# Optimization experiments

Hardware: AMD Instinct MI355X
Metric: run time of the kernel (lower is better)

Reference implementation:

```python
import jax, jax.numpy as jnp
import numpy as np


def setup_inputs() -> dict:
    key = jax.random.key(0)
    ks = jax.random.split(key, 7)
    B, C, H, W = 4, 64, 64, 64
    d = C // 8
    s = C ** -0.5  # 1x1-conv fan-in init scale
    x = jax.random.normal(ks[0], (B, C, H, W), jnp.float32)
    Wq = jax.random.normal(ks[1], (d, C), jnp.float32) * s
    bq = jnp.zeros((d,), jnp.float32)
    Wk = jax.random.normal(ks[2], (d, C), jnp.float32) * s
    bk = jnp.zeros((d,), jnp.float32)
    Wv = jax.random.normal(ks[3], (C, C), jnp.float32) * s
    bv = jnp.zeros((C,), jnp.float32)
    return {"x": x, "Wq": Wq, "bq": bq, "Wk": Wk, "bk": bk, "Wv": Wv, "bv": bv}


def reference(x, Wq, bq, Wk, bk, Wv, bv):
    B, C, H, W = x.shape
    N = H * W
    xf = x.reshape(B, C, N)                               # [B,C,N]
    # 1x1 convs == per-pixel channel matmuls
    q = jnp.einsum('dc,bcn->bnd', Wq, xf) + bq            # [B,N,d]
    k = jnp.einsum('dc,bcn->bnd', Wk, xf) + bk            # [B,N,d]
    v = jnp.einsum('ec,bcn->ben', Wv, xf) + bv[:, None]   # [B,C,N]
    # pairwise relative position offsets over flattened spatial grid
    idx = jnp.arange(N)
    col = (idx % W).astype(x.dtype)
    row = (idx // W).astype(x.dtype)
    col_diff = col[None, :] - col[:, None]                # [N,N], col_j - col_i
    row_diff = row[None, :] - row[:, None]                # [N,N]
    # scores = Q . (K + rel_pos folded into first two key channels)
    scores = jnp.einsum('bnd,bmd->bnm', q, k)             # [B,N,N]
    scores = scores + q[:, :, 0, None] * col_diff[None] + q[:, :, 1, None] * row_diff[None]
    attn = jax.nn.softmax(scores, axis=-1)                # softmax over keys
    out = jnp.einsum('bcm,bnm->bcn', v, attn)             # [B,C,N]
    return out.reshape(B, C, H, W)
```

## Files before the change

### kernel.cpp

```cpp
#include <hip/hip_runtime.h>

#define BB 4
#define CC 64
#define NN 4096

typedef __attribute__((ext_vector_type(8))) short short8;
typedef __attribute__((ext_vector_type(4))) float f32x4;
typedef __attribute__((ext_vector_type(4))) unsigned uint4v;

__device__ inline ushort f2bf(float x) {
    unsigned u = __float_as_uint(x);
    return (ushort)((u + 0x7fff + ((u >> 16) & 1)) >> 16);
}
__device__ inline float bf2f(ushort h) { return __uint_as_float(((unsigned)h) << 16); }

__device__ inline unsigned cvt_pk_bf16(float a, float b) {
    unsigned r;
    asm("v_cvt_pk_bf16_f32 %0, %1, %2" : "=v"(r) : "v"(a), "v"(b));
    return r;
}


__global__ __launch_bounds__(512) void qkv_kernel(
    const float* __restrict__ x,
    const float* __restrict__ Wq, const float* __restrict__ bq,
    const float* __restrict__ Wk, const float* __restrict__ bk,
    const float* __restrict__ Wv, const float* __restrict__ bv,
    ushort* __restrict__ qTp, ushort* __restrict__ kTp, ushort* __restrict__ vsw)
{
    __shared__ ushort vlds[32 * 68];
    const int blk = blockIdx.x;
    const int tid = threadIdx.x;

    if (blk < 32) {
        const int idx = blk * 512 + tid;
        const int b = idx >> 12, n = idx & (NN - 1);
        const float* xb = x + (size_t)b * CC * NN + n;
        float sq[8], sk[8];
#pragma unroll
        for (int d = 0; d < 8; ++d) { sq[d] = bq[d]; sk[d] = bk[d]; }
#pragma unroll 8
        for (int c = 0; c < CC; ++c) {
            const float xc = xb[c * NN];
#pragma unroll
            for (int d = 0; d < 8; ++d) {
                sq[d] += Wq[d * CC + c] * xc;
                sk[d] += Wk[d * CC + c] * xc;
            }
        }
        ushort hq[32], hk[32];
#pragma unroll
        for (int i = 0; i < 32; ++i) { hq[i] = 0; hk[i] = 0; }
#pragma unroll
        for (int d = 0; d < 8; ++d) { hq[d] = f2bf(sq[d]); hk[d] = f2bf(sk[d]); }
        hq[8]  = hq[0];
        hq[9]  = hq[1];
        hq[10] = f2bf(sq[0] - bf2f(hq[0]));
        hq[11] = f2bf(sq[1] - bf2f(hq[1]));
        const float col = (float)(n & 63), row = (float)(n >> 6);
        hk[8] = f2bf(col); hk[9] = f2bf(row); hk[10] = hk[8]; hk[11] = hk[9];

        uint4* dq = (uint4*)(qTp + (size_t)(b * NN + n) * 32);
        uint4* dk = (uint4*)(kTp + (size_t)(b * NN + n) * 32);
        const uint4* s4q = (const uint4*)hq;
        const uint4* s4k = (const uint4*)hk;
#pragma unroll
        for (int i = 0; i < 4; ++i) { dq[i] = s4q[i]; dk[i] = s4k[i]; }
        return;
    }

    const int w2 = blk - 32;
    const int bt = w2 >> 1, h = w2 & 1;
    const int b = bt >> 6, t = bt & 63;
    const int w = tid >> 6, j = tid & 63;
    const int n = t * 64 + j;
    const int e0 = __builtin_amdgcn_readfirstlane(h * 32 + w * 4);

    const float* xb = x + (size_t)b * CC * NN + n;
    float a0 = bv[e0], a1 = bv[e0 + 1], a2 = bv[e0 + 2], a3 = bv[e0 + 3];
#pragma unroll 8
    for (int c = 0; c < CC; ++c) {
        const float xc = xb[c * NN];
        a0 += Wv[(e0 + 0) * CC + c] * xc;
        a1 += Wv[(e0 + 1) * CC + c] * xc;
        a2 += Wv[(e0 + 2) * CC + c] * xc;
        a3 += Wv[(e0 + 3) * CC + c] * xc;
    }
    const int el0 = w * 4;
    vlds[(el0 + 0) * 68 + j] = f2bf(a0);
    vlds[(el0 + 1) * 68 + j] = f2bf(a1);
    vlds[(el0 + 2) * 68 + j] = f2bf(a2);
    vlds[(el0 + 3) * 68 + j] = f2bf(a3);
    __syncthreads();

    const int el = tid & 31;
    const int qd = (tid >> 5) & 3;
    const int sbh = tid >> 7;
    const int sb = sbh >> 1, hi = sbh & 1;
    const int j0 = sb * 32 + hi * 16 + qd * 4;
    const int eg = h * 32 + el;
    const uint2 val = *(const uint2*)(vlds + el * 68 + j0);
    const size_t tb = (size_t)(b * 64 + t) * 4096;
    *(uint2*)(vsw + tb + (size_t)(((sb * 4 + (eg >> 4)) * 64 + qd * 16 + (eg & 15)) * 8 + hi * 4)) = val;
}

__global__ __launch_bounds__(512) void attn_kernel(
    const ushort* __restrict__ qTp, const ushort* __restrict__ kTp,
    const ushort* __restrict__ vsw, float* __restrict__ out)
{
    const int blk = blockIdx.x;
    const int xcd = blk & 7, i8 = blk >> 3;
    const int b  = xcd >> 1;
    const int nq = (((xcd & 1) << 6) | i8) << 5;
    const int tid = threadIdx.x;
    const int wv = tid >> 6, lane = tid & 63;
    const int nn = lane & 15, quad = lane >> 4;

    __shared__ float Cb[8][1024];
    __shared__ float Mx[8][32];
    __shared__ float Db[8][32];
    __shared__ float dn[32];

    const short8 qf0 = *(const short8*)(qTp + ((size_t)(b * NN + nq + nn) * 32 + quad * 8));
    const short8 qf1 = *(const short8*)(qTp + ((size_t)(b * NN + nq + 16 + nn) * 32 + quad * 8));
    const ushort* kb = kTp + (size_t)b * NN * 32;

    float m0 = -1e30f, m1 = -1e30f;
    {
        const int t = wv * 8;
#pragma unroll
        for (int kg = 0; kg < 4; ++kg) {
            const short8 kf = *(const short8*)(kb + ((size_t)(t * 64 + kg * 16 + nn) * 32 + quad * 8));
            const f32x4 S0 = __builtin_amdgcn_mfma_f32_16x16x32_bf16(kf, qf0, (f32x4){0.f,0.f,0.f,0.f}, 0, 0, 0);
            const f32x4 S1 = __builtin_amdgcn_mfma_f32_16x16x32_bf16(kf, qf1, (f32x4){0.f,0.f,0.f,0.f}, 0, 0, 0);
            m0 = fmaxf(m0, fmaxf(fmaxf(S0[0], S0[1]), fmaxf(S0[2], S0[3])));
            m1 = fmaxf(m1, fmaxf(fmaxf(S1[0], S1[1]), fmaxf(S1[2], S1[3])));
        }
        m0 = fmaxf(m0, __shfl_xor(m0, 16, 64));
        m0 = fmaxf(m0, __shfl_xor(m0, 32, 64));
        m1 = fmaxf(m1, __shfl_xor(m1, 16, 64));
        m1 = fmaxf(m1, __shfl_xor(m1, 32, 64));
    }
    f32x4 nM0 = {-m0, -m0, -m0, -m0};
    f32x4 nM1 = {-m1, -m1, -m1, -m1};

    f32x4 acc0[4], acc1[4];
#pragma unroll
    for (int g = 0; g < 4; ++g) {
        acc0[g] = (f32x4){0.f,0.f,0.f,0.f};
        acc1[g] = (f32x4){0.f,0.f,0.f,0.f};
    }
    float dl0 = 0.f, dl1 = 0.f;

    for (int t8 = 0; t8 < 8; ++t8) {
        const int t = wv * 8 + t8;
        f32x4 s0[4], s1[4];
#pragma unroll
        for (int kg = 0; kg < 4; ++kg) {
            const short8 kf = *(const short8*)(kb + ((size_t)(t * 64 + kg * 16 + nn) * 32 + quad * 8));
            s0[kg] = __builtin_amdgcn_mfma_f32_16x16x32_bf16(kf, qf0, nM0, 0, 0, 0);
            s1[kg] = __builtin_amdgcn_mfma_f32_16x16x32_bf16(kf, qf1, nM1, 0, 0, 0);
        }
        float r0 = fmaxf(fmaxf(s0[0][0], s0[0][1]), fmaxf(s0[0][2], s0[0][3]));
        float r1 = fmaxf(fmaxf(s1[0][0], s1[0][1]), fmaxf(s1[0][2], s1[0][3]));
#pragma unroll
        for (int kg = 1; kg < 4; ++kg) {
            r0 = fmaxf(r0, fmaxf(fmaxf(s0[kg][0], s0[kg][1]), fmaxf(s0[kg][2], s0[kg][3])));
            r1 = fmaxf(r1, fmaxf(fmaxf(s1[kg][0], s1[kg][1]), fmaxf(s1[kg][2], s1[kg][3])));
        }
        r0 = fmaxf(r0, __shfl_xor(r0, 16, 64));
        r0 = fmaxf(r0, __shfl_xor(r0, 32, 64));
        r1 = fmaxf(r1, __shfl_xor(r1, 16, 64));
        r1 = fmaxf(r1, __shfl_xor(r1, 32, 64));

        if (__any((r0 > 25.f) || (r1 > 25.f))) {
            const float d0 = fmaxf(r0, 0.f), d1 = fmaxf(r1, 0.f);
            const float e0 = __expf(-d0), e1 = __expf(-d1);
            m0 += d0; m1 += d1;
            nM0 = (f32x4){-m0, -m0, -m0, -m0};
            nM1 = (f32x4){-m1, -m1, -m1, -m1};
            dl0 *= e0; dl1 *= e1;
            f32x4 e0v, e1v;
#pragma unroll
            for (int rr = 0; rr < 4; ++rr) {
                e0v[rr] = __shfl(e0, quad * 4 + rr, 64);
                e1v[rr] = __shfl(e1, quad * 4 + rr, 64);
            }
#pragma unroll
            for (int g = 0; g < 4; ++g) { acc0[g] *= e0v; acc1[g] *= e1v; }
            const f32x4 dv0 = {d0, d0, d0, d0}, dv1 = {d1, d1, d1, d1};
#pragma unroll
            for (int kg = 0; kg < 4; ++kg) { s0[kg] -= dv0; s1[kg] -= dv1; }
        }

        unsigned pw0[8], pw1[8];
#pragma unroll
        for (int kg = 0; kg < 4; ++kg) {
            const float w00 = __expf(s0[kg][0]), w01 = __expf(s0[kg][1]);
            const float w02 = __expf(s0[kg][2]), w03 = __expf(s0[kg][3]);
            const float w10 = __expf(s1[kg][0]), w11 = __expf(s1[kg][1]);
            const float w12 = __expf(s1[kg][2]), w13 = __expf(s1[kg][3]);
            dl0 += (w00 + w01) + (w02 + w03);
            dl1 += (w10 + w11) + (w12 + w13);
            pw0[2 * kg]     = cvt_pk_bf16(w00, w01);
            pw0[2 * kg + 1] = cvt_pk_bf16(w02, w03);
            pw1[2 * kg]     = cvt_pk_bf16(w10, w11);
            pw1[2 * kg + 1] = cvt_pk_bf16(w12, w13);
        }
        const uint4v u00 = {pw0[0], pw0[1], pw0[2], pw0[3]};
        const uint4v u01 = {pw0[4], pw0[5], pw0[6], pw0[7]};
        const uint4v u10 = {pw1[0], pw1[1], pw1[2], pw1[3]};
        const uint4v u11 = {pw1[4], pw1[5], pw1[6], pw1[7]};
        const short8 a00 = __builtin_bit_cast(short8, u00);
        const short8 a01 = __builtin_bit_cast(short8, u01);
        const short8 a10 = __builtin_bit_cast(short8, u10);
        const short8 a11 = __builtin_bit_cast(short8, u11);

        const ushort* vb = vsw + (size_t)(b * 64 + t) * 4096;
#pragma unroll
        for (int g = 0; g < 4; ++g) {
            const short8 vf = *(const short8*)(vb + g * 512 + lane * 8);
            acc0[g] = __builtin_amdgcn_mfma_f32_16x16x32_bf16(a00, vf, acc0[g], 0, 0, 0);
            acc1[g] = __builtin_amdgcn_mfma_f32_16x16x32_bf16(a10, vf, acc1[g], 0, 0, 0);
        }
#pragma unroll
        for (int g = 0; g < 4; ++g) {
            const short8 vf = *(const short8*)(vb + 2048 + g * 512 + lane * 8);
            acc0[g] = __builtin_amdgcn_mfma_f32_16x16x32_bf16(a01, vf, acc0[g], 0, 0, 0);
            acc1[g] = __builtin_amdgcn_mfma_f32_16x16x32_bf16(a11, vf, acc1[g], 0, 0, 0);
        }
    }

    if (quad == 0) { Mx[wv][nn] = m0; Mx[wv][16 + nn] = m1; }
    __syncthreads();
    float M0 = Mx[0][nn], M1 = Mx[0][16 + nn];
#pragma unroll
    for (int w = 1; w < 8; ++w) { M0 = fmaxf(M0, Mx[w][nn]); M1 = fmaxf(M1, Mx[w][16 + nn]); }
    const float g0 = __expf(m0 - M0), g1 = __expf(m1 - M1);
    dl0 *= g0; dl1 *= g1;
    f32x4 g0v, g1v;
#pragma unroll
    for (int rr = 0; rr < 4; ++rr) {
        g0v[rr] = __shfl(g0, quad * 4 + rr, 64);
        g1v[rr] = __shfl(g1, quad * 4 + rr, 64);
    }
#pragma unroll
    for (int g = 0; g < 4; ++g) { acc0[g] *= g0v; acc1[g] *= g1v; }

    dl0 += __shfl_xor(dl0, 16, 64); dl0 += __shfl_xor(dl0, 32, 64);
    dl1 += __shfl_xor(dl1, 16, 64); dl1 += __shfl_xor(dl1, 32, 64);
    if (quad == 0) { Db[wv][nn] = dl0; Db[wv][16 + nn] = dl1; }

#pragma unroll
    for (int g = 0; g < 4; ++g)
#pragma unroll
        for (int r = 0; r < 4; ++r)
            Cb[wv][(g * 4 + r) * 64 + lane] = acc0[g][r];
    __syncthreads();

    if (tid < 32) {
        float s = Db[0][tid];
#pragma unroll
        for (int w = 1; w < 8; ++w) s += Db[w][tid];
        dn[tid] = s;
    }
    __syncthreads();

#pragma unroll
    for (int it = 0; it < 2; ++it) {
        const int e = tid + it * 512;
        const int q = e & 15, c = e >> 4;
        const int src = ((c >> 4) * 4 + (q & 3)) * 64 + (q >> 2) * 16 + (c & 15);
        float v = Cb[0][src];
#pragma unroll
        for (int w = 1; w < 8; ++w) v += Cb[w][src];
        out[(size_t)(b * CC + c) * NN + nq + q] = v / dn[q];
    }
    __syncthreads();

#pragma unroll
    for (int g = 0; g < 4; ++g)
#pragma unroll
        for (int r = 0; r < 4; ++r)
            Cb[wv][(g * 4 + r) * 64 + lane] = acc1[g][r];
    __syncthreads();

#pragma unroll
    for (int it = 0; it < 2; ++it) {
        const int e = tid + it * 512;
        const int q = e & 15, c = e >> 4;
        const int src = ((c >> 4) * 4 + (q & 3)) * 64 + (q >> 2) * 16 + (c & 15);
        float v = Cb[0][src];
#pragma unroll
        for (int w = 1; w < 8; ++w) v += Cb[w][src];
        out[(size_t)(b * CC + c) * NN + nq + 16 + q] = v / dn[16 + q];
    }
}

extern "C" void kernel_launch(void* const* d_in, const int* in_sizes, int n_in,
                              void* d_out, int out_size, void* d_ws, size_t ws_size,
                              hipStream_t stream) {
    const float* x  = (const float*)d_in[0];
    const float* Wq = (const float*)d_in[1];
    const float* bq = (const float*)d_in[2];
    const float* Wk = (const float*)d_in[3];
    const float* bk = (const float*)d_in[4];
    const float* Wv = (const float*)d_in[5];
    const float* bv = (const float*)d_in[6];
    float* out = (float*)d_out;

    ushort* ws  = (ushort*)d_ws;
    ushort* qTp = ws;
    ushort* kTp = ws + (size_t)BB * NN * 32;
    ushort* vsw = ws + (size_t)2 * BB * NN * 32;

    qkv_kernel<<<544, 512, 0, stream>>>(x, Wq, bq, Wk, bk, Wv, bv, qTp, kTp, vsw);
    attn_kernel<<<512, 512, 0, stream>>>(qTp, kTp, vsw, out);
}
```

Baseline: 113.9 us.

## Process 64 queries per attention block to reuse K and V loads

Each attention block now handles 64 query rows (four 16-row tiles) instead of 32, and the grid is halved from 512 to 256 blocks. K and V fragments loaded per key tile are reused across twice as many query tiles, which halves global K/V traffic per query. The cost is double the accumulator registers per thread, and 256 blocks may underfill a GPU with 256 CUs running one 512-thread block each. The epilogue reductions also now run sequentially over four tiles, adding barriers.

New measurement: 111.3 us. 2.3% less time.

```diff
diff --git a/kernel.cpp b/kernel.cpp
--- a/kernel.cpp
+++ b/kernel.cpp
@@ -111,189 +111,191 @@
     const int blk = blockIdx.x;
     const int xcd = blk & 7, i8 = blk >> 3;
     const int b  = xcd >> 1;
-    const int nq = (((xcd & 1) << 6) | i8) << 5;
+    const int nq = (((xcd & 1) << 5) | i8) << 6;
     const int tid = threadIdx.x;
     const int wv = tid >> 6, lane = tid & 63;
     const int nn = lane & 15, quad = lane >> 4;
 
     __shared__ float Cb[8][1024];
-    __shared__ float Mx[8][32];
-    __shared__ float Db[8][32];
-    __shared__ float dn[32];
-
-    const short8 qf0 = *(const short8*)(qTp + ((size_t)(b * NN + nq + nn) * 32 + quad * 8));
-    const short8 qf1 = *(const short8*)(qTp + ((size_t)(b * NN + nq + 16 + nn) * 32 + quad * 8));
+    __shared__ float Mx[8][64];
+    __shared__ float Db[8][64];
+    __shared__ float dn[64];
+
+    short8 qf[4];
+#pragma unroll
+    for (int qt = 0; qt < 4; ++qt)
+        qf[qt] = *(const short8*)(qTp + ((size_t)(b * NN + nq + qt * 16 + nn) * 32 + quad * 8));
     const ushort* kb = kTp + (size_t)b * NN * 32;
 
-    float m0 = -1e30f, m1 = -1e30f;
+    float m[4] = {-1e30f, -1e30f, -1e30f, -1e30f};
     {
         const int t = wv * 8;
 #pragma unroll
-        for (int kg = 0; kg < 4; ++kg) {
-            const short8 kf = *(const short8*)(kb + ((size_t)(t * 64 + kg * 16 + nn) * 32 + quad * 8));
-            const f32x4 S0 = __builtin_amdgcn_mfma_f32_16x16x32_bf16(kf, qf0, (f32x4){0.f,0.f,0.f,0.f}, 0, 0, 0);
-            const f32x4 S1 = __builtin_amdgcn_mfma_f32_16x16x32_bf16(kf, qf1, (f32x4){0.f,0.f,0.f,0.f}, 0, 0, 0);
-            m0 = fmaxf(m0, fmaxf(fmaxf(S0[0], S0[1]), fmaxf(S0[2], S0[3])));
-            m1 = fmaxf(m1, fmaxf(fmaxf(S1[0], S1[1]), fmaxf(S1[2], S1[3])));
-        }
-        m0 = fmaxf(m0, __shfl_xor(m0, 16, 64));
-        m0 = fmaxf(m0, __shfl_xor(m0, 32, 64));
-        m1 = fmaxf(m1, __shfl_xor(m1, 16, 64));
-        m1 = fmaxf(m1, __shfl_xor(m1, 32, 64));
-    }
-    f32x4 nM0 = {-m0, -m0, -m0, -m0};
-    f32x4 nM1 = {-m1, -m1, -m1, -m1};
-
-    f32x4 acc0[4], acc1[4];
-#pragma unroll
-    for (int g = 0; g < 4; ++g) {
-        acc0[g] = (f32x4){0.f,0.f,0.f,0.f};
-        acc1[g] = (f32x4){0.f,0.f,0.f,0.f};
-    }
-    float dl0 = 0.f, dl1 = 0.f;
+        for (int p = 0; p < 2; ++p) {
+            const int q0 = 2 * p, q1 = 2 * p + 1;
+#pragma unroll
+            for (int kg = 0; kg < 4; ++kg) {
+                const short8 kf = *(const short8*)(kb + ((size_t)(t * 64 + kg * 16 + nn) * 32 + quad * 8));
+                const f32x4 S0 = __builtin_amdgcn_mfma_f32_16x16x32_bf16(kf, qf[q0], (f32x4){0.f,0.f,0.f,0.f}, 0, 0, 0);
+                const f32x4 S1 = __builtin_amdgcn_mfma_f32_16x16x32_bf16(kf, qf[q1], (f32x4){0.f,0.f,0.f,0.f}, 0, 0, 0);
+                m[q0] = fmaxf(m[q0], fmaxf(fmaxf(S0[0], S0[1]), fmaxf(S0[2], S0[3])));
+                m[q1] = fmaxf(m[q1], fmaxf(fmaxf(S1[0], S1[1]), fmaxf(S1[2], S1[3])));
+            }
+        }
+#pragma unroll
+        for (int qt = 0; qt < 4; ++qt) {
+            m[qt] = fmaxf(m[qt], __shfl_xor(m[qt], 16, 64));
+            m[qt] = fmaxf(m[qt], __shfl_xor(m[qt], 32, 64));
+        }
+    }
+    f32x4 nM[4];
+#pragma unroll
+    for (int qt = 0; qt < 4; ++qt) nM[qt] = (f32x4){-m[qt], -m[qt], -m[qt], -m[qt]};
+
+    f32x4 acc[4][4];
+#pragma unroll
+    for (int qt = 0; qt < 4; ++qt)
+#pragma unroll
+        for (int g = 0; g < 4; ++g) acc[qt][g] = (f32x4){0.f,0.f,0.f,0.f};
+    float dl[4] = {0.f, 0.f, 0.f, 0.f};
 
     for (int t8 = 0; t8 < 8; ++t8) {
         const int t = wv * 8 + t8;
-        f32x4 s0[4], s1[4];
-#pragma unroll
-        for (int kg = 0; kg < 4; ++kg) {
-            const short8 kf = *(const short8*)(kb + ((size_t)(t * 64 + kg * 16 + nn) * 32 + quad * 8));
-            s0[kg] = __builtin_amdgcn_mfma_f32_16x16x32_bf16(kf, qf0, nM0, 0, 0, 0);
-            s1[kg] = __builtin_amdgcn_mfma_f32_16x16x32_bf16(kf, qf1, nM1, 0, 0, 0);
-        }
-        float r0 = fmaxf(fmaxf(s0[0][0], s0[0][1]), fmaxf(s0[0][2], s0[0][3]));
-        float r1 = fmaxf(fmaxf(s1[0][0], s1[0][1]), fmaxf(s1[0][2], s1[0][3]));
-#pragma unroll
-        for (int kg = 1; kg < 4; ++kg) {
-            r0 = fmaxf(r0, fmaxf(fmaxf(s0[kg][0], s0[kg][1]), fmaxf(s0[kg][2], s0[kg][3])));
-            r1 = fmaxf(r1, fmaxf(fmaxf(s1[kg][0], s1[kg][1]), fmaxf(s1[kg][2], s1[kg][3])));
-        }
-        r0 = fmaxf(r0, __shfl_xor(r0, 16, 64));
-        r0 = fmaxf(r0, __shfl_xor(r0, 32, 64));
-        r1 = fmaxf(r1, __shfl_xor(r1, 16, 64));
-        r1 = fmaxf(r1, __shfl_xor(r1, 32, 64));
-
-        if (__any((r0 > 25.f) || (r1 > 25.f))) {
-            const float d0 = fmaxf(r0, 0.f), d1 = fmaxf(r1, 0.f);
-            const float e0 = __expf(-d0), e1 = __expf(-d1);
-            m0 += d0; m1 += d1;
-            nM0 = (f32x4){-m0, -m0, -m0, -m0};
-            nM1 = (f32x4){-m1, -m1, -m1, -m1};
-            dl0 *= e0; dl1 *= e1;
-            f32x4 e0v, e1v;
-#pragma unroll
-            for (int rr = 0; rr < 4; ++rr) {
-                e0v[rr] = __shfl(e0, quad * 4 + rr, 64);
-                e1v[rr] = __shfl(e1, quad * 4 + rr, 64);
-            }
-#pragma unroll
-            for (int g = 0; g < 4; ++g) { acc0[g] *= e0v; acc1[g] *= e1v; }
-            const f32x4 dv0 = {d0, d0, d0, d0}, dv1 = {d1, d1, d1, d1};
-#pragma unroll
-            for (int kg = 0; kg < 4; ++kg) { s0[kg] -= dv0; s1[kg] -= dv1; }
-        }
-
-        unsigned pw0[8], pw1[8];
-#pragma unroll
-        for (int kg = 0; kg < 4; ++kg) {
-            const float w00 = __expf(s0[kg][0]), w01 = __expf(s0[kg][1]);
-            const float w02 = __expf(s0[kg][2]), w03 = __expf(s0[kg][3]);
-            const float w10 = __expf(s1[kg][0]), w11 = __expf(s1[kg][1]);
-            const float w12 = __expf(s1[kg][2]), w13 = __expf(s1[kg][3]);
-            dl0 += (w00 + w01) + (w02 + w03);
-            dl1 += (w10 + w11) + (w12 + w13);
-            pw0[2 * kg]     = cvt_pk_bf16(w00, w01);
-            pw0[2 * kg + 1] = cvt_pk_bf16(w02, w03);
-            pw1[2 * kg]     = cvt_pk_bf16(w10, w11);
-            pw1[2 * kg + 1] = cvt_pk_bf16(w12, w13);
-        }
-        const uint4v u00 = {pw0[0], pw0[1], pw0[2], pw0[3]};
-        const uint4v u01 = {pw0[4], pw0[5], pw0[6], pw0[7]};
-        const uint4v u10 = {pw1[0], pw1[1], pw1[2], pw1[3]};
-        const uint4v u11 = {pw1[4], pw1[5], pw1[6], pw1[7]};
-        const short8 a00 = __builtin_bit_cast(short8, u00);
-        const short8 a01 = __builtin_bit_cast(short8, u01);
-        const short8 a10 = __builtin_bit_cast(short8, u10);
-        const short8 a11 = __builtin_bit_cast(short8, u11);
-
         const ushort* vb = vsw + (size_t)(b * 64 + t) * 4096;
-#pragma unroll
-        for (int g = 0; g < 4; ++g) {
-            const short8 vf = *(const short8*)(vb + g * 512 + lane * 8);
-            acc0[g] = __builtin_amdgcn_mfma_f32_16x16x32_bf16(a00, vf, acc0[g], 0, 0, 0);
-            acc1[g] = __builtin_amdgcn_mfma_f32_16x16x32_bf16(a10, vf, acc1[g], 0, 0, 0);
-        }
-#pragma unroll
-        for (int g = 0; g < 4; ++g) {
-            const short8 vf = *(const short8*)(vb + 2048 + g * 512 + lane * 8);
-            acc0[g] = __builtin_amdgcn_mfma_f32_16x16x32_bf16(a01, vf, acc0[g], 0, 0, 0);
-            acc1[g] = __builtin_amdgcn_mfma_f32_16x16x32_bf16(a11, vf, acc1[g], 0, 0, 0);
-        }
-    }
-
-    if (quad == 0) { Mx[wv][nn] = m0; Mx[wv][16 + nn] = m1; }
+
+#pragma unroll
+        for (int p = 0; p < 2; ++p) {
+            const int q0 = 2 * p, q1 = 2 * p + 1;
+            f32x4 s0[4], s1[4];
+#pragma unroll
+            for (int kg = 0; kg < 4; ++kg) {
+                const short8 kf = *(const short8*)(kb + ((size_t)(t * 64 + kg * 16 + nn) * 32 + quad * 8));
+                s0[kg] = __builtin_amdgcn_mfma_f32_16x16x32_bf16(kf, qf[q0], nM[q0], 0, 0, 0);
+                s1[kg] = __builtin_amdgcn_mfma_f32_16x16x32_bf16(kf, qf[q1], nM[q1], 0, 0, 0);
+            }
+            float r0 = fmaxf(fmaxf(s0[0][0], s0[0][1]), fmaxf(s0[0][2], s0[0][3]));
+            float r1 = fmaxf(fmaxf(s1[0][0], s1[0][1]), fmaxf(s1[0][2], s1[0][3]));
+#pragma unroll
+            for (int kg = 1; kg < 4; ++kg) {
+                r0 = fmaxf(r0, fmaxf(fmaxf(s0[kg][0], s0[kg][1]), fmaxf(s0[kg][2], s0[kg][3])));
+                r1 = fmaxf(r1, fmaxf(fmaxf(s1[kg][0], s1[kg][1]), fmaxf(s1[kg][2], s1[kg][3])));
+            }
+            r0 = fmaxf(r0, __shfl_xor(r0, 16, 64));
+            r0 = fmaxf(r0, __shfl_xor(r0, 32, 64));
+            r1 = fmaxf(r1, __shfl_xor(r1, 16, 64));
+            r1 = fmaxf(r1, __shfl_xor(r1, 32, 64));
+
+            if (__any((r0 > 25.f) || (r1 > 25.f))) {
+                const float d0 = fmaxf(r0, 0.f), d1 = fmaxf(r1, 0.f);
+                const float e0 = __expf(-d0), e1 = __expf(-d1);
+                m[q0] += d0; m[q1] += d1;
+                nM[q0] = (f32x4){-m[q0], -m[q0], -m[q0], -m[q0]};
+                nM[q1] = (f32x4){-m[q1], -m[q1], -m[q1], -m[q1]};
+                dl[q0] *= e0; dl[q1] *= e1;
+                f32x4 e0v, e1v;
+#pragma unroll
+                for (int rr = 0; rr < 4; ++rr) {
+                    e0v[rr] = __shfl(e0, quad * 4 + rr, 64);
+                    e1v[rr] = __shfl(e1, quad * 4 + rr, 64);
+                }
+#pragma unroll
+                for (int g = 0; g < 4; ++g) { acc[q0][g] *= e0v; acc[q1][g] *= e1v; }
+                const f32x4 dv0 = {d0, d0, d0, d0}, dv1 = {d1, d1, d1, d1};
+#pragma unroll
+                for (int kg = 0; kg < 4; ++kg) { s0[kg] -= dv0; s1[kg] -= dv1; }
+            }
+
+            unsigned pw0[8], pw1[8];
+#pragma unroll
+            for (int kg = 0; kg < 4; ++kg) {
+                const float w00 = __expf(s0[kg][0]), w01 = __expf(s0[kg][1]);
+                const float w02 = __expf(s0[kg][2]), w03 = __expf(s0[kg][3]);
+                const float w10 = __expf(s1[kg][0]), w11 = __expf(s1[kg][1]);
+                const float w12 = __expf(s1[kg][2]), w13 = __expf(s1[kg][3]);
+                dl[q0] += (w00 + w01) + (w02 + w03);
+                dl[q1] += (w10 + w11) + (w12 + w13);
+                pw0[2 * kg]     = cvt_pk_bf16(w00, w01);
+                pw0[2 * kg + 1] = cvt_pk_bf16(w02, w03);
+                pw1[2 * kg]     = cvt_pk_bf16(w10, w11);
+                pw1[2 * kg + 1] = cvt_pk_bf16(w12, w13);
+            }
+            const uint4v u00 = {pw0[0], pw0[1], pw0[2], pw0[3]};
+            const uint4v u01 = {pw0[4], pw0[5], pw0[6], pw0[7]};
+            const uint4v u10 = {pw1[0], pw1[1], pw1[2], pw1[3]};
+            const uint4v u11 = {pw1[4], pw1[5], pw1[6], pw1[7]};
+            const short8 a00 = __builtin_bit_cast(short8, u00);
+            const short8 a01 = __builtin_bit_cast(short8, u01);
+            const short8 a10 = __builtin_bit_cast(short8, u10);
+            const short8 a11 = __builtin_bit_cast(short8, u11);
+
+#pragma unroll
+            for (int g = 0; g < 4; ++g) {
+                const short8 vf = *(const short8*)(vb + g * 512 + lane * 8);
+                acc[q0][g] = __builtin_amdgcn_mfma_f32_16x16x32_bf16(a00, vf, acc[q0][g], 0, 0, 0);
+                acc[q1][g] = __builtin_amdgcn_mfma_f32_16x16x32_bf16(a10, vf, acc[q1][g], 0, 0, 0);
+            }
+#pragma unroll
+            for (int g = 0; g < 4; ++g) {
+                const short8 vf = *(const short8*)(vb + 2048 + g * 512 + lane * 8);
+                acc[q0][g] = __builtin_amdgcn_mfma_f32_16x16x32_bf16(a01, vf, acc[q0][g], 0, 0, 0);
+                acc[q1][g] = __builtin_amdgcn_mfma_f32_16x16x32_bf16(a11, vf, acc[q1][g], 0, 0, 0);
+            }
+        }
+    }
+
+    if (quad == 0) {
+#pragma unroll
+        for (int qt = 0; qt < 4; ++qt) Mx[wv][qt * 16 + nn] = m[qt];
+    }
     __syncthreads();
-    float M0 = Mx[0][nn], M1 = Mx[0][16 + nn];
-#pragma unroll
-    for (int w = 1; w < 8; ++w) { M0 = fmaxf(M0, Mx[w][nn]); M1 = fmaxf(M1, Mx[w][16 + nn]); }
-    const float g0 = __expf(m0 - M0), g1 = __expf(m1 - M1);
-    dl0 *= g0; dl1 *= g1;
-    f32x4 g0v, g1v;
-#pragma unroll
-    for (int rr = 0; rr < 4; ++rr) {
-        g0v[rr] = __shfl(g0, quad * 4 + rr, 64);
-        g1v[rr] = __shfl(g1, quad * 4 + rr, 64);
-    }
-#pragma unroll
-    for (int g = 0; g < 4; ++g) { acc0[g] *= g0v; acc1[g] *= g1v; }
-
-    dl0 += __shfl_xor(dl0, 16, 64); dl0 += __shfl_xor(dl0, 32, 64);
-    dl1 += __shfl_xor(dl1, 16, 64); dl1 += __shfl_xor(dl1, 32, 64);
-    if (quad == 0) { Db[wv][nn] = dl0; Db[wv][16 + nn] = dl1; }
-
-#pragma unroll
-    for (int g = 0; g < 4; ++g)
-#pragma unroll
-        for (int r = 0; r < 4; ++r)
-            Cb[wv][(g * 4 + r) * 64 + lane] = acc0[g][r];
-    __syncthreads();
-
-    if (tid < 32) {
-        float s = Db[0][tid];
-#pragma unroll
-        for (int w = 1; w < 8; ++w) s += Db[w][tid];
-        dn[tid] = s;
-    }
-    __syncthreads();
-
-#pragma unroll
-    for (int it = 0; it < 2; ++it) {
-        const int e = tid + it * 512;
-        const int q = e & 15, c = e >> 4;
-        const int src = ((c >> 4) * 4 + (q & 3)) * 64 + (q >> 2) * 16 + (c & 15);
-        float v = Cb[0][src];
-#pragma unroll
-        for (int w = 1; w < 8; ++w) v += Cb[w][src];
-        out[(size_t)(b * CC + c) * NN + nq + q] = v / dn[q];
-    }
-    __syncthreads();
-
-#pragma unroll
-    for (int g = 0; g < 4; ++g)
-#pragma unroll
-        for (int r = 0; r < 4; ++r)
-            Cb[wv][(g * 4 + r) * 64 + lane] = acc1[g][r];
-    __syncthreads();
-
-#pragma unroll
-    for (int it = 0; it < 2; ++it) {
-        const int e = tid + it * 512;
-        const int q = e & 15, c = e >> 4;
-        const int src = ((c >> 4) * 4 + (q & 3)) * 64 + (q >> 2) * 16 + (c & 15);
-        float v = Cb[0][src];
-#pragma unroll
-        for (int w = 1; w < 8; ++w) v += Cb[w][src];
-        out[(size_t)(b * CC + c) * NN + nq + 16 + q] = v / dn[16 + q];
+#pragma unroll
+    for (int qt = 0; qt < 4; ++qt) {
+        float M = Mx[0][qt * 16 + nn];
+#pragma unroll
+        for (int w = 1; w < 8; ++w) M = fmaxf(M, Mx[w][qt * 16 + nn]);
+        const float gq = __expf(m[qt] - M);
+        dl[qt] *= gq;
+        f32x4 gv;
+#pragma unroll
+        for (int rr = 0; rr < 4; ++rr) gv[rr] = __shfl(gq, quad * 4 + rr, 64);
+#pragma unroll
+        for (int g = 0; g < 4; ++g) acc[qt][g] *= gv;
+        dl[qt] += __shfl_xor(dl[qt], 16, 64);
+        dl[qt] += __shfl_xor(dl[qt], 32, 64);
+    }
+    if (quad == 0) {
+#pragma unroll
+        for (int qt = 0; qt < 4; ++qt) Db[wv][qt * 16 + nn] = dl[qt];
+    }
+
+#pragma unroll
+    for (int qt = 0; qt < 4; ++qt) {
+#pragma unroll
+        for (int g = 0; g < 4; ++g)
+#pragma unroll
+            for (int r = 0; r < 4; ++r)
+                Cb[wv][(g * 4 + r) * 64 + lane] = acc[qt][g][r];
+        __syncthreads();
+        if (qt == 0) {
+            if (tid < 64) {
+                float s = Db[0][tid];
+#pragma unroll
+                for (int w = 1; w < 8; ++w) s += Db[w][tid];
+                dn[tid] = s;
+            }
+            __syncthreads();
+        }
+#pragma unroll
+        for (int it = 0; it < 2; ++it) {
+            const int e = tid + it * 512;
+            const int q = e & 15, c = e >> 4;
+            const int src = ((c >> 4) * 4 + (q & 3)) * 64 + (q >> 2) * 16 + (c & 15);
+            float v = Cb[0][src];
+#pragma unroll
+            for (int w = 1; w < 8; ++w) v += Cb[w][src];
+            out[(size_t)(b * CC + c) * NN + nq + qt * 16 + q] = v / dn[qt * 16 + q];
+        }
+        __syncthreads();
     }
 }
 
@@ -315,5 +317,5 @@
     ushort* vsw = ws + (size_t)2 * BB * NN * 32;
 
     qkv_kernel<<<544, 512, 0, stream>>>(x, Wq, bq, Wk, bk, Wv, bv, qTp, kTp, vsw);
-    attn_kernel<<<512, 512, 0, stream>>>(qTp, kTp, vsw, out);
-}
+    attn_kernel<<<256, 512, 0, stream>>>(qTp, kTp, vsw, out);
+}
```

## Split attention key range across 16 waves per block with two-phase reduction

Applied to the files above, without the earlier changes.

Doubles the attention block size to 1024 threads, so each wave handles 4 key tiles instead of 8 and the per-query key range is split across 16 waves. The cross-wave reduction of partial outputs is restructured into two passes through the existing 8-slot shared buffer, so shared memory does not grow, at the cost of extra barriers. The aim is more parallelism and latency hiding per query tile, with a shorter serial loop per wave. The risks are higher register pressure under the 1024-thread launch bound and more synchronization overhead in the epilogue.

After: 121.2 us. +6.4%, slower.

```diff
diff --git a/kernel.cpp b/kernel.cpp
--- a/kernel.cpp
+++ b/kernel.cpp
@@ -104,7 +104,7 @@
     *(uint2*)(vsw + tb + (size_t)(((sb * 4 + (eg >> 4)) * 64 + qd * 16 + (eg & 15)) * 8 + hi * 4)) = val;
 }
 
-__global__ __launch_bounds__(512) void attn_kernel(
+__global__ __launch_bounds__(1024) void attn_kernel(
     const ushort* __restrict__ qTp, const ushort* __restrict__ kTp,
     const ushort* __restrict__ vsw, float* __restrict__ out)
 {
@@ -117,8 +117,8 @@
     const int nn = lane & 15, quad = lane >> 4;
 
     __shared__ float Cb[8][1024];
-    __shared__ float Mx[8][32];
-    __shared__ float Db[8][32];
+    __shared__ float Mx[16][32];
+    __shared__ float Db[16][32];
     __shared__ float dn[32];
 
     const short8 qf0 = *(const short8*)(qTp + ((size_t)(b * NN + nq + nn) * 32 + quad * 8));
@@ -127,7 +127,7 @@
 
     float m0 = -1e30f, m1 = -1e30f;
     {
-        const int t = wv * 8;
+        const int t = wv * 4;
 #pragma unroll
         for (int kg = 0; kg < 4; ++kg) {
             const short8 kf = *(const short8*)(kb + ((size_t)(t * 64 + kg * 16 + nn) * 32 + quad * 8));
@@ -152,8 +152,10 @@
     }
     float dl0 = 0.f, dl1 = 0.f;
 
-    for (int t8 = 0; t8 < 8; ++t8) {
-        const int t = wv * 8 + t8;
+    for (int t8 = 0; t8 < 4; ++t8) {
+        const int t = wv * 4 + t8;
+        const ushort* vb = vsw + (size_t)(b * 64 + t) * 4096;
+
         f32x4 s0[4], s1[4];
 #pragma unroll
         for (int kg = 0; kg < 4; ++kg) {
@@ -207,27 +209,19 @@
             pw1[2 * kg]     = cvt_pk_bf16(w10, w11);
             pw1[2 * kg + 1] = cvt_pk_bf16(w12, w13);
         }
-        const uint4v u00 = {pw0[0], pw0[1], pw0[2], pw0[3]};
-        const uint4v u01 = {pw0[4], pw0[5], pw0[6], pw0[7]};
-        const uint4v u10 = {pw1[0], pw1[1], pw1[2], pw1[3]};
-        const uint4v u11 = {pw1[4], pw1[5], pw1[6], pw1[7]};
-        const short8 a00 = __builtin_bit_cast(short8, u00);
-        const short8 a01 = __builtin_bit_cast(short8, u01);
-        const short8 a10 = __builtin_bit_cast(short8, u10);
-        const short8 a11 = __builtin_bit_cast(short8, u11);
-
-        const ushort* vb = vsw + (size_t)(b * 64 + t) * 4096;
-#pragma unroll
-        for (int g = 0; g < 4; ++g) {
-            const short8 vf = *(const short8*)(vb + g * 512 + lane * 8);
-            acc0[g] = __builtin_amdgcn_mfma_f32_16x16x32_bf16(a00, vf, acc0[g], 0, 0, 0);
-            acc1[g] = __builtin_amdgcn_mfma_f32_16x16x32_bf16(a10, vf, acc1[g], 0, 0, 0);
-        }
-#pragma unroll
-        for (int g = 0; g < 4; ++g) {
-            const short8 vf = *(const short8*)(vb + 2048 + g * 512 + lane * 8);
-            acc0[g] = __builtin_amdgcn_mfma_f32_16x16x32_bf16(a01, vf, acc0[g], 0, 0, 0);
-            acc1[g] = __builtin_amdgcn_mfma_f32_16x16x32_bf16(a11, vf, acc1[g], 0, 0, 0);
+
+#pragma unroll
+        for (int sb = 0; sb < 2; ++sb) {
+            const uint4v u0 = {pw0[4 * sb], pw0[4 * sb + 1], pw0[4 * sb + 2], pw0[4 * sb + 3]};
+            const uint4v u1 = {pw1[4 * sb], pw1[4 * sb + 1], pw1[4 * sb + 2], pw1[4 * sb + 3]};
+            const short8 af0 = __builtin_bit_cast(short8, u0);
+            const short8 af1 = __builtin_bit_cast(short8, u1);
+#pragma unroll
+            for (int g = 0; g < 4; ++g) {
+                const short8 vf = *(const short8*)(vb + sb * 2048 + g * 512 + lane * 8);
+                acc0[g] = __builtin_amdgcn_mfma_f32_16x16x32_bf16(af0, vf, acc0[g], 0, 0, 0);
+                acc1[g] = __builtin_amdgcn_mfma_f32_16x16x32_bf16(af1, vf, acc1[g], 0, 0, 0);
+            }
         }
     }
 
@@ -235,7 +229,7 @@
     __syncthreads();
     float M0 = Mx[0][nn], M1 = Mx[0][16 + nn];
 #pragma unroll
-    for (int w = 1; w < 8; ++w) { M0 = fmaxf(M0, Mx[w][nn]); M1 = fmaxf(M1, Mx[w][16 + nn]); }
+    for (int w = 1; w < 16; ++w) { M0 = fmaxf(M0, Mx[w][nn]); M1 = fmaxf(M1, Mx[w][16 + nn]); }
     const float g0 = __expf(m0 - M0), g1 = __expf(m1 - M1);
     dl0 *= g0; dl1 *= g1;
     f32x4 g0v, g1v;
@@ -251,50 +245,63 @@
     dl1 += __shfl_xor(dl1, 16, 64); dl1 += __shfl_xor(dl1, 32, 64);
     if (quad == 0) { Db[wv][nn] = dl0; Db[wv][16 + nn] = dl1; }
 
-#pragma unroll
-    for (int g = 0; g < 4; ++g)
-#pragma unroll
-        for (int r = 0; r < 4; ++r)
-            Cb[wv][(g * 4 + r) * 64 + lane] = acc0[g][r];
-    __syncthreads();
-
+    const int eq = tid & 15, ec = (tid >> 4) & 63;
+    const int src = ((ec >> 4) * 4 + (eq & 3)) * 64 + (eq >> 2) * 16 + (ec & 15);
+
+    if (wv < 8) {
+#pragma unroll
+        for (int g = 0; g < 4; ++g)
+#pragma unroll
+            for (int r = 0; r < 4; ++r)
+                Cb[wv][(g * 4 + r) * 64 + lane] = acc0[g][r];
+    }
+    __syncthreads();
     if (tid < 32) {
         float s = Db[0][tid];
 #pragma unroll
-        for (int w = 1; w < 8; ++w) s += Db[w][tid];
+        for (int w = 1; w < 16; ++w) s += Db[w][tid];
         dn[tid] = s;
     }
-    __syncthreads();
-
-#pragma unroll
-    for (int it = 0; it < 2; ++it) {
-        const int e = tid + it * 512;
-        const int q = e & 15, c = e >> 4;
-        const int src = ((c >> 4) * 4 + (q & 3)) * 64 + (q >> 2) * 16 + (c & 15);
-        float v = Cb[0][src];
-#pragma unroll
-        for (int w = 1; w < 8; ++w) v += Cb[w][src];
-        out[(size_t)(b * CC + c) * NN + nq + q] = v / dn[q];
-    }
-    __syncthreads();
-
-#pragma unroll
-    for (int g = 0; g < 4; ++g)
-#pragma unroll
-        for (int r = 0; r < 4; ++r)
-            Cb[wv][(g * 4 + r) * 64 + lane] = acc1[g][r];
-    __syncthreads();
-
-#pragma unroll
-    for (int it = 0; it < 2; ++it) {
-        const int e = tid + it * 512;
-        const int q = e & 15, c = e >> 4;
-        const int src = ((c >> 4) * 4 + (q & 3)) * 64 + (q >> 2) * 16 + (c & 15);
-        float v = Cb[0][src];
-#pragma unroll
-        for (int w = 1; w < 8; ++w) v += Cb[w][src];
-        out[(size_t)(b * CC + c) * NN + nq + 16 + q] = v / dn[16 + q];
-    }
+    float v0 = Cb[0][src];
+#pragma unroll
+    for (int w = 1; w < 8; ++w) v0 += Cb[w][src];
+    __syncthreads();
+    if (wv >= 8) {
+#pragma unroll
+        for (int g = 0; g < 4; ++g)
+#pragma unroll
+            for (int r = 0; r < 4; ++r)
+                Cb[wv - 8][(g * 4 + r) * 64 + lane] = acc0[g][r];
+    }
+    __syncthreads();
+#pragma unroll
+    for (int w = 0; w < 8; ++w) v0 += Cb[w][src];
+    out[(size_t)(b * CC + ec) * NN + nq + eq] = v0 / dn[eq];
+    __syncthreads();
+
+    if (wv < 8) {
+#pragma unroll
+        for (int g = 0; g < 4; ++g)
+#pragma unroll
+            for (int r = 0; r < 4; ++r)
+                Cb[wv][(g * 4 + r) * 64 + lane] = acc1[g][r];
+    }
+    __syncthreads();
+    float v1 = Cb[0][src];
+#pragma unroll
+    for (int w = 1; w < 8; ++w) v1 += Cb[w][src];
+    __syncthreads();
+    if (wv >= 8) {
+#pragma unroll
+        for (int g = 0; g < 4; ++g)
+#pragma unroll
+            for (int r = 0; r < 4; ++r)
+                Cb[wv - 8][(g * 4 + r) * 64 + lane] = acc1[g][r];
+    }
+    __syncthreads();
+#pragma unroll
+    for (int w = 0; w < 8; ++w) v1 += Cb[w][src];
+    out[(size_t)(b * CC + ec) * NN + nq + 16 + eq] = v1 / dn[16 + eq];
 }
 
 extern "C" void kernel_launch(void* const* d_in, const int* in_sizes, int n_in,
@@ -315,5 +322,5 @@
     ushort* vsw = ws + (size_t)2 * BB * NN * 32;
 
     qkv_kernel<<<544, 512, 0, stream>>>(x, Wq, bq, Wk, bk, Wv, bv, qTp, kTp, vsw);
-    attn_kernel<<<512, 512, 0, stream>>>(qTp, kTp, vsw, out);
-}
+    attn_kernel<<<512, 1024, 0, stream>>>(qTp, kTp, vsw, out);
+}
```
